# Optimization experiments

Hardware: AMD Instinct MI355X
Metric: run time of the kernel (lower is better)

Reference implementation:

```python
import jax, jax.numpy as jnp
import numpy as np

NEG_INF = -1.0e9  # matches torch code's masked fill value


def setup_inputs() -> dict:
    key = jax.random.key(0)
    k1, k2, k3, k4 = jax.random.split(key, 4)
    n, q, s, d, v = 8, 4096, 4096, 64, 64
    return {
        "queries_nqd": jax.random.normal(k1, (n, q, d), dtype=jnp.float32),
        "keys_nsd": jax.random.normal(k2, (n, s, d), dtype=jnp.float32),
        "values_nsv": jax.random.normal(k3, (n, s, v), dtype=jnp.float32),
        "attention_mask_nqs": jax.random.randint(k4, (n, q, s), 0, 2).astype(jnp.bool_),
    }


def reference(queries_nqd, keys_nsd, values_nsv, attention_mask_nqs):
    d = queries_nqd.shape[-1]
    scale = 1.0 / jnp.sqrt(jnp.asarray(d, dtype=queries_nqd.dtype))
    # [n,q,s] = [n,q,d] @ [n,d,s]
    scores_nqs = jnp.einsum("nqd,nsd->nqs", queries_nqd, keys_nsd) * scale
    scores_nqs = jnp.where(attention_mask_nqs, scores_nqs, jnp.asarray(NEG_INF, scores_nqs.dtype))
    probs_nqs = jax.nn.softmax(scores_nqs, axis=-1)
    # dropout p=0.0 (eval) -> identity
    return jnp.einsum("nqs,nsv->nqv", probs_nqs, values_nsv)
```

## Files before the change

### kernel.cpp

```cpp
#include <hip/hip_runtime.h>
#include <hip/hip_bf16.h>


#define NHEADS 8
#define QLEN   4096
#define SLEN   4096
#define DDIM   64
#define VDIM   64
#define SBLK   64
#define QBLK   128
#define NCHUNK (SLEN / SBLK)

typedef __bf16          bf16x4 __attribute__((ext_vector_type(4)));
typedef __bf16          bf16x8 __attribute__((ext_vector_type(8)));
typedef float           f32x4  __attribute__((ext_vector_type(4)));
typedef float           f32x16 __attribute__((ext_vector_type(16)));
typedef unsigned int    u32x4  __attribute__((ext_vector_type(4)));
typedef unsigned short  u16x4  __attribute__((ext_vector_type(4)));

#define KSWZ(s) (((s) & 7) << 4)
#define VSWZ(v) ((((v) >> 2) & 7) << 4)
#define PSWZ(q) (((q) & 3) << 4)
#define CLAMPC(c) ((c) < NCHUNK ? (c) : NCHUNK - 1)

#define LDS_BARRIER() do {                                          \
  asm volatile("s_waitcnt lgkmcnt(0)" ::: "memory");                \
  __builtin_amdgcn_s_barrier();                                     \
  __builtin_amdgcn_sched_barrier(0);                                \
} while (0)

__device__ __forceinline__ f32x16 zero16() {
  f32x16 z;
#pragma unroll
  for (int i = 0; i < 16; ++i) z[i] = 0.f;
  return z;
}

__device__ __forceinline__ int detect_mfmt(const unsigned char* __restrict__ M) {
  const int lane = threadIdx.x & 63;
  u32x4 w = *((const u32x4*)M + lane);
  unsigned o = w[0] | w[1] | w[2] | w[3];
  unsigned comb = ((o & 0x00FFFF00u) ? 1u : 0u) | ((o & 0x000000FFu) ? 2u : 0u);
  comb |= __shfl_xor((int)comb, 1);  comb |= __shfl_xor((int)comb, 2);
  comb |= __shfl_xor((int)comb, 4);  comb |= __shfl_xor((int)comb, 8);
  comb |= __shfl_xor((int)comb, 16); comb |= __shfl_xor((int)comb, 32);
  return ((comb & 1u) == 0u) ? 1 : (((comb & 2u) == 0u) ? 2 : 0);
}

template<bool U8>
__global__ __launch_bounds__(512, 2)
void attn_fwd(const float* __restrict__ Qg, const float* __restrict__ Kg,
              const float* __restrict__ Vg, const unsigned char* __restrict__ Mg,
              float* __restrict__ Og)
{
  __shared__ __align__(16) unsigned short Ksh[2][64 * 64];
  __shared__ __align__(16) unsigned short Vsh[2][64 * 64];
  __shared__ __align__(16) unsigned short Psh[8][32 * 32];
  __shared__ __align__(16) float mO[4][32][68];
  __shared__            float mM[4][2][32];

  {
    const int mfmt = detect_mfmt(Mg);
    if (U8 ? (mfmt != 0) : (mfmt == 0)) return;
  }

  const int tid   = threadIdx.x;
  const int wave  = tid >> 6;
  const int lane  = tid & 63;
  const int qtile = wave & 3;
  const int shalf = wave >> 2;
  const int lq    = lane & 31;
  const int h     = lane >> 5;

  const int head = blockIdx.x;
  const int qblk = blockIdx.y;

  const float* Qp = Qg + ((size_t)head * QLEN + (size_t)qblk * QBLK) * DDIM;
  const float* Kp = Kg + (size_t)head * SLEN * DDIM;
  const float* Vp = Vg + (size_t)head * SLEN * VDIM;
  float* Op = Og + ((size_t)head * QLEN + (size_t)qblk * QBLK) * DDIM;

  const float QSCALE = 0.125f * 1.44269504f;
  const int qrow = qtile * 32 + lq;
  bf16x8 qf[4];
#pragma unroll
  for (int kd = 0; kd < 4; ++kd) {
    const float* qp = Qp + (size_t)qrow * DDIM + 16 * kd + 8 * h;
    f32x4 a = *(const f32x4*)qp;
    f32x4 b = *(const f32x4*)(qp + 4);
    bf16x8 t;
#pragma unroll
    for (int j = 0; j < 4; ++j) { t[j] = (__bf16)(a[j] * QSCALE); t[4 + j] = (__bf16)(b[j] * QSCALE); }
    qf[kd] = t;
  }

  const size_t mbase = ((size_t)head * QLEN + (size_t)qblk * QBLK + qrow) * SLEN
                     + (size_t)shalf * 32;
  const unsigned char* mrow8  = Mg + mbase;
  const unsigned*      mrow32 = (const unsigned*)Mg + mbase;

  f32x16 oacc[2];
  oacc[0] = zero16(); oacc[1] = zero16();
  float m_run = -INFINITY;
  float l_run = 0.f;

  f32x4 kpA[2], vpA[2], kpB[2], vpB[2];
  unsigned m8A[4],  m8B[4];
  u32x4    m32A[4], m32B[4];

#define PREFETCH_KV(C, KP, VP)                                                 \
  _Pragma("unroll")                                                            \
  for (int it = 0; it < 2; ++it) {                                             \
    int srow = (tid >> 4) + it * 32;                                           \
    int d0   = (tid & 15) * 4;                                                 \
    size_t gs = (size_t)(CLAMPC(C) * SBLK + srow);                             \
    KP[it] = *(const f32x4*)(Kp + gs * DDIM + d0);                             \
    VP[it] = *(const f32x4*)(Vp + gs * VDIM + d0);                             \
  }

#define WRITE_KV(BUF, KP, VP)                                                  \
  _Pragma("unroll")                                                            \
  for (int it = 0; it < 2; ++it) {                                             \
    int srow = (tid >> 4) + it * 32;                                           \
    int d0   = (tid & 15) * 4;                                                 \
    bf16x4 kb;                                                                 \
    _Pragma("unroll") for (int j = 0; j < 4; ++j) kb[j] = (__bf16)KP[it][j];   \
    int koff = (srow * 128 + d0 * 2) ^ KSWZ(srow);                             \
    *(u16x4*)((char*)Ksh[BUF] + koff) = __builtin_bit_cast(u16x4, kb);         \
    _Pragma("unroll")                                                          \
    for (int j = 0; j < 4; ++j) {                                              \
      int v = d0 + j;                                                          \
      unsigned short b = __builtin_bit_cast(unsigned short, (__bf16)VP[it][j]); \
      int voff = (v * 128 + srow * 2) ^ VSWZ(v);                               \
      *(unsigned short*)((char*)Vsh[BUF] + voff) = b;                          \
    }                                                                          \
  }

#define LOAD_MASK(M8, M32, C)                                                  \
  if constexpr (U8) {                                                          \
    _Pragma("unroll")                                                          \
    for (int st = 0; st < 4; ++st)                                             \
      M8[st] = *(const unsigned*)(mrow8 + (size_t)CLAMPC(C) * SBLK + 8 * st + 4 * h); \
  } else {                                                                     \
    _Pragma("unroll")                                                          \
    for (int st = 0; st < 4; ++st)                                             \
      M32[st] = *(const u32x4*)(mrow32 + (size_t)CLAMPC(C) * SBLK + 8 * st + 4 * h); \
  }

#define CHUNK_BODY(C, CUR, KPF, VPF, KPW, VPW, M8U, M32U) {                    \
  PREFETCH_KV((C) + 2, KPF, VPF);                                              \
       \
  f32x16 sacc = zero16();                                                      \
  __builtin_amdgcn_s_setprio(1);                                               \
  _Pragma("unroll")                                                            \
  for (int kd = 0; kd < 4; ++kd) {                                             \
    int srow = shalf * 32 + lq;                                                \
    int off = (srow * 128 + (32 * kd + 16 * h)) ^ KSWZ(srow);                  \
    bf16x8 kf = *(const bf16x8*)((const char*)Ksh[CUR] + off);                 \
    sacc = __builtin_amdgcn_mfma_f32_32x32x16_bf16(kf, qf[kd], sacc, 0, 0, 0); \
  }                                                                            \
  __builtin_amdgcn_s_setprio(0);                                               \
               \
  float vals[4][4];                                                            \
  float mloc = -INFINITY;                                                      \
  _Pragma("unroll")                                                            \
  for (int st = 0; st < 4; ++st) {                                             \
    bool keep[4];                                                              \
    if constexpr (U8) {                                                        \
      _Pragma("unroll")                                                        \
      for (int r = 0; r < 4; ++r) keep[r] = ((M8U[st] >> (8 * r)) & 0xFFu) != 0u; \
    } else {                                                                   \
      _Pragma("unroll")                                                        \
      for (int r = 0; r < 4; ++r) keep[r] = M32U[st][r] != 0u;                 \
    }                                                                          \
    _Pragma("unroll")                                                          \
    for (int r = 0; r < 4; ++r) {                                              \
      float v = keep[r] ? sacc[4 * st + r] : -1.0e9f;                          \
      vals[st][r] = v;                                                         \
      mloc = fmaxf(mloc, v);                                                   \
    }                                                                          \
  }                                                                            \
  LOAD_MASK(M8U, M32U, (C) + 2);            \
  mloc = fmaxf(mloc, __shfl_xor(mloc, 32));                                    \
      \
  if (!__all(mloc <= m_run + 8.0f)) {                                          \
    float m_new = fmaxf(m_run, mloc);                                          \
    float alpha = __builtin_amdgcn_exp2f(m_run - m_new);                       \
    l_run *= alpha;                                                            \
    _Pragma("unroll")                                                          \
    for (int vt = 0; vt < 2; ++vt) {                                           \
      _Pragma("unroll")                                                        \
      for (int r = 0; r < 16; ++r) oacc[vt][r] *= alpha;                       \
    }                                                                          \
    m_run = m_new;                                                             \
  }                                                                            \
  float lsum = 0.f;                                                            \
  _Pragma("unroll")                                                            \
  for (int st = 0; st < 4; ++st) {                                             \
    bf16x4 pb;                                                                 \
    _Pragma("unroll")                                                          \
    for (int r = 0; r < 4; ++r) {                                              \
      float p = __builtin_amdgcn_exp2f(vals[st][r] - m_run);                   \
      lsum += p;                                                               \
      pb[r] = (__bf16)p;                                                       \
    }                                                                          \
    int poff = (lq * 64 + (16 * st + 8 * h)) ^ PSWZ(lq);                       \
    *(unsigned long long*)((char*)Psh[wave] + poff) =                          \
        __builtin_bit_cast(unsigned long long, pb);                            \
  }                                                                            \
  lsum += __shfl_xor(lsum, 32);                                                \
  l_run += lsum;                                                               \
               \
  __builtin_amdgcn_s_setprio(1);                                               \
  _Pragma("unroll")                                                            \
  for (int ks2 = 0; ks2 < 2; ++ks2) {                                          \
    int poff = (lq * 64 + (32 * ks2 + 16 * h)) ^ PSWZ(lq);                     \
    bf16x8 pf = *(const bf16x8*)((const char*)Psh[wave] + poff);               \
    _Pragma("unroll")                                                          \
    for (int vt = 0; vt < 2; ++vt) {                                           \
      int vrow = vt * 32 + lq;                                                 \
      int voff = (vrow * 128 + (64 * shalf + 32 * ks2 + 16 * h)) ^ VSWZ(vrow); \
      bf16x8 vf = *(const bf16x8*)((const char*)Vsh[CUR] + voff);              \
      oacc[vt] = __builtin_amdgcn_mfma_f32_32x32x16_bf16(vf, pf, oacc[vt], 0, 0, 0); \
    }                                                                          \
  }                                                                            \
  __builtin_amdgcn_s_setprio(0);                                               \
  WRITE_KV((CUR) ^ 1, KPW, VPW);         \
  LDS_BARRIER();                                                               \
}

  PREFETCH_KV(0, kpA, vpA);
  LOAD_MASK(m8A, m32A, 0);
  PREFETCH_KV(1, kpB, vpB);
  LOAD_MASK(m8B, m32B, 1);
  WRITE_KV(0, kpA, vpA);
  LDS_BARRIER();

  for (int cc = 0; cc < NCHUNK; cc += 2) {
    CHUNK_BODY(cc,     0, kpA, vpA, kpB, vpB, m8A, m32A);
    CHUNK_BODY(cc + 1, 1, kpB, vpB, kpA, vpA, m8B, m32B);
  }

  if (shalf == 1) {
#pragma unroll
    for (int vt = 0; vt < 2; ++vt) {
#pragma unroll
      for (int st = 0; st < 4; ++st) {
        int v0 = 32 * vt + 8 * st + 4 * h;
        f32x4 o;
#pragma unroll
        for (int r = 0; r < 4; ++r) o[r] = oacc[vt][4 * st + r];
        *(f32x4*)&mO[qtile][lq][v0] = o;
      }
    }
    if (h == 0) {
      mM[qtile][0][lq] = m_run;
      mM[qtile][1][lq] = l_run;
    }
  }
  LDS_BARRIER();
  if (shalf == 0) {
    float m1 = mM[qtile][0][lq];
    float l1 = mM[qtile][1][lq];
    float mm = fmaxf(m_run, m1);
    float a0 = __builtin_amdgcn_exp2f(m_run - mm);
    float a1 = __builtin_amdgcn_exp2f(m1 - mm);
    float inv = 1.0f / (l_run * a0 + l1 * a1);
    float* orow = Op + (size_t)qrow * VDIM;
#pragma unroll
    for (int vt = 0; vt < 2; ++vt) {
#pragma unroll
      for (int st = 0; st < 4; ++st) {
        int v0 = 32 * vt + 8 * st + 4 * h;
        f32x4 o1 = *(const f32x4*)&mO[qtile][lq][v0];
        f32x4 o;
#pragma unroll
        for (int r = 0; r < 4; ++r) o[r] = (oacc[vt][4 * st + r] * a0 + o1[r] * a1) * inv;
        *(f32x4*)(orow + v0) = o;
      }
    }
  }
#undef PREFETCH_KV
#undef WRITE_KV
#undef LOAD_MASK
#undef CHUNK_BODY
}

extern "C" void kernel_launch(void* const* d_in, const int* in_sizes, int n_in,
                              void* d_out, int out_size, void* d_ws, size_t ws_size,
                              hipStream_t stream) {
  const float* Qg = (const float*)d_in[0];
  const float* Kg = (const float*)d_in[1];
  const float* Vg = (const float*)d_in[2];
  const unsigned char* Mg = (const unsigned char*)d_in[3];
  float* Og = (float*)d_out;

  dim3 grid(NHEADS, QLEN / QBLK);
  dim3 block(512);
  attn_fwd<true ><<<grid, block, 0, stream>>>(Qg, Kg, Vg, Mg, Og);
  attn_fwd<false><<<grid, block, 0, stream>>>(Qg, Kg, Vg, Mg, Og);
}
```

Baseline: 150.2 us.

## Process 128-key phases and pass P through cross-lane shuffles instead of LDS

Doubles the per-phase key block to 128, so each barrier covers two 32-key tiles per wave and the number of LDS barriers and K/V staging rounds is halved. The softmax probabilities are packed into bf16 pairs and exchanged between lane halves with __shfl_xor to build the MFMA B operand directly, removing the per-wave P scratch buffer in LDS. The final merge buffers reuse the K/V shared arrays. The cost is more registers (8 prefetched K/V vectors and 8 mask words per buffer) and a shallower prefetch distance of one phase instead of two chunks, which could reduce occupancy or expose load latency.

```diff
diff --git a/kernel.cpp b/kernel.cpp
--- a/kernel.cpp
+++ b/kernel.cpp
@@ -7,9 +7,9 @@
 #define SLEN   4096
 #define DDIM   64
 #define VDIM   64
-#define SBLK   64
+#define PBLK   128
 #define QBLK   128
-#define NCHUNK (SLEN / SBLK)
+#define NPHASE (SLEN / PBLK)
 
 typedef __bf16          bf16x4 __attribute__((ext_vector_type(4)));
 typedef __bf16          bf16x8 __attribute__((ext_vector_type(8)));
@@ -20,8 +20,7 @@
 
 #define KSWZ(s) (((s) & 7) << 4)
 #define VSWZ(v) ((((v) >> 2) & 7) << 4)
-#define PSWZ(q) (((q) & 3) << 4)
-#define CLAMPC(c) ((c) < NCHUNK ? (c) : NCHUNK - 1)
+#define CLAMPP(p) ((p) < NPHASE ? (p) : NPHASE - 1)
 
 #define LDS_BARRIER() do {                                          \
   asm volatile("s_waitcnt lgkmcnt(0)" ::: "memory");                \
@@ -34,6 +33,13 @@
 #pragma unroll
   for (int i = 0; i < 16; ++i) z[i] = 0.f;
   return z;
+}
+
+__device__ __forceinline__ unsigned short bfb(float x) {
+  return __builtin_bit_cast(unsigned short, (__bf16)x);
+}
+__device__ __forceinline__ unsigned pk2(float a, float b) {
+  return (unsigned)bfb(a) | ((unsigned)bfb(b) << 16);
 }
 
 __device__ __forceinline__ int detect_mfmt(const unsigned char* __restrict__ M) {
@@ -53,11 +59,8 @@
               const float* __restrict__ Vg, const unsigned char* __restrict__ Mg,
               float* __restrict__ Og)
 {
-  __shared__ __align__(16) unsigned short Ksh[2][64 * 64];
-  __shared__ __align__(16) unsigned short Vsh[2][64 * 64];
-  __shared__ __align__(16) unsigned short Psh[8][32 * 32];
-  __shared__ __align__(16) float mO[4][32][68];
-  __shared__            float mM[4][2][32];
+  __shared__ __align__(16) unsigned short Ksh[2][128 * 64];
+  __shared__ __align__(16) unsigned short Vsh[2][64 * 128];
 
   {
     const int mfmt = detect_mfmt(Mg);
@@ -94,8 +97,7 @@
     qf[kd] = t;
   }
 
-  const size_t mbase = ((size_t)head * QLEN + (size_t)qblk * QBLK + qrow) * SLEN
-                     + (size_t)shalf * 32;
+  const size_t mbase = ((size_t)head * QLEN + (size_t)qblk * QBLK + qrow) * SLEN;
   const unsigned char* mrow8  = Mg + mbase;
   const unsigned*      mrow32 = (const unsigned*)Mg + mbase;
 
@@ -104,74 +106,87 @@
   float m_run = -INFINITY;
   float l_run = 0.f;
 
-  f32x4 kpA[2], vpA[2], kpB[2], vpB[2];
-  unsigned m8A[4],  m8B[4];
-  u32x4    m32A[4], m32B[4];
-
-#define PREFETCH_KV(C, KP, VP)                                                 \
-  _Pragma("unroll")                                                            \
-  for (int it = 0; it < 2; ++it) {                                             \
-    int srow = (tid >> 4) + it * 32;                                           \
-    int d0   = (tid & 15) * 4;                                                 \
-    size_t gs = (size_t)(CLAMPC(C) * SBLK + srow);                             \
-    KP[it] = *(const f32x4*)(Kp + gs * DDIM + d0);                             \
-    VP[it] = *(const f32x4*)(Vp + gs * VDIM + d0);                             \
-  }
-
-#define WRITE_KV(BUF, KP, VP)                                                  \
-  _Pragma("unroll")                                                            \
-  for (int it = 0; it < 2; ++it) {                                             \
-    int srow = (tid >> 4) + it * 32;                                           \
+  f32x4 kp0, kp1, kp2, kp3, vp0, vp1, vp2, vp3;
+  unsigned m8A[8],  m8B[8];
+  u32x4    m32A[8], m32B[8];
+
+#define PREFETCH_KV(P)                                                         \
+  {                                                                            \
+    size_t b_ = (size_t)CLAMPP(P) * PBLK;                                      \
+    int sr_ = tid >> 4, d0_ = (tid & 15) * 4;                                  \
+    kp0 = *(const f32x4*)(Kp + (b_ + sr_     ) * DDIM + d0_);                  \
+    kp1 = *(const f32x4*)(Kp + (b_ + sr_ + 32) * DDIM + d0_);                  \
+    kp2 = *(const f32x4*)(Kp + (b_ + sr_ + 64) * DDIM + d0_);                  \
+    kp3 = *(const f32x4*)(Kp + (b_ + sr_ + 96) * DDIM + d0_);                  \
+    vp0 = *(const f32x4*)(Vp + (b_ + sr_     ) * VDIM + d0_);                  \
+    vp1 = *(const f32x4*)(Vp + (b_ + sr_ + 32) * VDIM + d0_);                  \
+    vp2 = *(const f32x4*)(Vp + (b_ + sr_ + 64) * VDIM + d0_);                  \
+    vp3 = *(const f32x4*)(Vp + (b_ + sr_ + 96) * VDIM + d0_);                  \
+  }
+
+#define WRITE_ONE(BUF, KP, VP, IT)                                             \
+  {                                                                            \
+    int srow = (tid >> 4) + (IT) * 32;                                         \
     int d0   = (tid & 15) * 4;                                                 \
     bf16x4 kb;                                                                 \
-    _Pragma("unroll") for (int j = 0; j < 4; ++j) kb[j] = (__bf16)KP[it][j];   \
+    _Pragma("unroll") for (int j = 0; j < 4; ++j) kb[j] = (__bf16)KP[j];       \
     int koff = (srow * 128 + d0 * 2) ^ KSWZ(srow);                             \
     *(u16x4*)((char*)Ksh[BUF] + koff) = __builtin_bit_cast(u16x4, kb);         \
     _Pragma("unroll")                                                          \
     for (int j = 0; j < 4; ++j) {                                              \
       int v = d0 + j;                                                          \
-      unsigned short b = __builtin_bit_cast(unsigned short, (__bf16)VP[it][j]); \
-      int voff = (v * 128 + srow * 2) ^ VSWZ(v);                               \
+      unsigned short b = __builtin_bit_cast(unsigned short, (__bf16)VP[j]);    \
+      int voff = (v * 256 + srow * 2) ^ VSWZ(v);                               \
       *(unsigned short*)((char*)Vsh[BUF] + voff) = b;                          \
     }                                                                          \
   }
 
-#define LOAD_MASK(M8, M32, C)                                                  \
+#define WRITE_KV(BUF)                                                          \
+  WRITE_ONE(BUF, kp0, vp0, 0) WRITE_ONE(BUF, kp1, vp1, 1)                      \
+  WRITE_ONE(BUF, kp2, vp2, 2) WRITE_ONE(BUF, kp3, vp3, 3)
+
+#define LOAD_MASK(M8, M32, P)                                                  \
   if constexpr (U8) {                                                          \
     _Pragma("unroll")                                                          \
-    for (int st = 0; st < 4; ++st)                                             \
-      M8[st] = *(const unsigned*)(mrow8 + (size_t)CLAMPC(C) * SBLK + 8 * st + 4 * h); \
+    for (int st2 = 0; st2 < 2; ++st2)                                          \
+      _Pragma("unroll")                                                        \
+      for (int st = 0; st < 4; ++st)                                           \
+        M8[4 * st2 + st] = *(const unsigned*)(mrow8 + (size_t)CLAMPP(P) * PBLK \
+                           + 64 * shalf + 32 * st2 + 8 * st + 4 * h);          \
   } else {                                                                     \
     _Pragma("unroll")                                                          \
-    for (int st = 0; st < 4; ++st)                                             \
-      M32[st] = *(const u32x4*)(mrow32 + (size_t)CLAMPC(C) * SBLK + 8 * st + 4 * h); \
-  }
-
-#define CHUNK_BODY(C, CUR, KPF, VPF, KPW, VPW, M8U, M32U) {                    \
-  PREFETCH_KV((C) + 2, KPF, VPF);                                              \
-       \
+    for (int st2 = 0; st2 < 2; ++st2)                                          \
+      _Pragma("unroll")                                                        \
+      for (int st = 0; st < 4; ++st)                                           \
+        M32[4 * st2 + st] = *(const u32x4*)(mrow32 + (size_t)CLAMPP(P) * PBLK  \
+                           + 64 * shalf + 32 * st2 + 8 * st + 4 * h);          \
+  }
+
+#define TILE(CUR, ST2, MU8, MU32) {                                            \
+                       \
   f32x16 sacc = zero16();                                                      \
+  int srow_ = 64 * shalf + 32 * (ST2) + lq;                                    \
   __builtin_amdgcn_s_setprio(1);                                               \
   _Pragma("unroll")                                                            \
   for (int kd = 0; kd < 4; ++kd) {                                             \
-    int srow = shalf * 32 + lq;                                                \
-    int off = (srow * 128 + (32 * kd + 16 * h)) ^ KSWZ(srow);                  \
+    int off = (srow_ * 128 + (32 * kd + 16 * h)) ^ KSWZ(srow_);                \
     bf16x8 kf = *(const bf16x8*)((const char*)Ksh[CUR] + off);                 \
     sacc = __builtin_amdgcn_mfma_f32_32x32x16_bf16(kf, qf[kd], sacc, 0, 0, 0); \
   }                                                                            \
   __builtin_amdgcn_s_setprio(0);                                               \
-               \
+                     \
   float vals[4][4];                                                            \
   float mloc = -INFINITY;                                                      \
   _Pragma("unroll")                                                            \
   for (int st = 0; st < 4; ++st) {                                             \
     bool keep[4];                                                              \
     if constexpr (U8) {                                                        \
-      _Pragma("unroll")                                                        \
-      for (int r = 0; r < 4; ++r) keep[r] = ((M8U[st] >> (8 * r)) & 0xFFu) != 0u; \
+      unsigned w_ = MU8[4 * (ST2) + st];                                       \
+      _Pragma("unroll")                                                        \
+      for (int r = 0; r < 4; ++r) keep[r] = ((w_ >> (8 * r)) & 0xFFu) != 0u;   \
     } else {                                                                   \
       _Pragma("unroll")                                                        \
-      for (int r = 0; r < 4; ++r) keep[r] = M32U[st][r] != 0u;                 \
+      for (int r = 0; r < 4; ++r) keep[r] = MU32[4 * (ST2) + st][r] != 0u;     \
     }                                                                          \
     _Pragma("unroll")                                                          \
     for (int r = 0; r < 4; ++r) {                                              \
@@ -180,88 +195,102 @@
       mloc = fmaxf(mloc, v);                                                   \
     }                                                                          \
   }                                                                            \
-  LOAD_MASK(M8U, M32U, (C) + 2);            \
   mloc = fmaxf(mloc, __shfl_xor(mloc, 32));                                    \
-      \
-  if (!__all(mloc <= m_run + 8.0f)) {                                          \
+  if (!__all(mloc <= m_run + 8.0f)) {                   \
     float m_new = fmaxf(m_run, mloc);                                          \
     float alpha = __builtin_amdgcn_exp2f(m_run - m_new);                       \
     l_run *= alpha;                                                            \
     _Pragma("unroll")                                                          \
-    for (int vt = 0; vt < 2; ++vt) {                                           \
+    for (int vt = 0; vt < 2; ++vt)                                             \
       _Pragma("unroll")                                                        \
       for (int r = 0; r < 16; ++r) oacc[vt][r] *= alpha;                       \
-    }                                                                          \
     m_run = m_new;                                                             \
   }                                                                            \
+                 \
   float lsum = 0.f;                                                            \
+  unsigned wlo[4], whi[4];                                                     \
   _Pragma("unroll")                                                            \
   for (int st = 0; st < 4; ++st) {                                             \
-    bf16x4 pb;                                                                 \
-    _Pragma("unroll")                                                          \
-    for (int r = 0; r < 4; ++r) {                                              \
-      float p = __builtin_amdgcn_exp2f(vals[st][r] - m_run);                   \
-      lsum += p;                                                               \
-      pb[r] = (__bf16)p;                                                       \
-    }                                                                          \
-    int poff = (lq * 64 + (16 * st + 8 * h)) ^ PSWZ(lq);                       \
-    *(unsigned long long*)((char*)Psh[wave] + poff) =                          \
-        __builtin_bit_cast(unsigned long long, pb);                            \
+    float p0 = __builtin_amdgcn_exp2f(vals[st][0] - m_run);                    \
+    float p1 = __builtin_amdgcn_exp2f(vals[st][1] - m_run);                    \
+    float p2 = __builtin_amdgcn_exp2f(vals[st][2] - m_run);                    \
+    float p3 = __builtin_amdgcn_exp2f(vals[st][3] - m_run);                    \
+    lsum += (p0 + p1) + (p2 + p3);                                             \
+    wlo[st] = pk2(p0, p1);                                                     \
+    whi[st] = pk2(p2, p3);                                                     \
   }                                                                            \
   lsum += __shfl_xor(lsum, 32);                                                \
   l_run += lsum;                                                               \
-               \
-  __builtin_amdgcn_s_setprio(1);                                               \
+   \
+   \
+   \
   _Pragma("unroll")                                                            \
   for (int ks2 = 0; ks2 < 2; ++ks2) {                                          \
-    int poff = (lq * 64 + (32 * ks2 + 16 * h)) ^ PSWZ(lq);                     \
-    bf16x8 pf = *(const bf16x8*)((const char*)Psh[wave] + poff);               \
+    unsigned slo = h ? wlo[2 * ks2] : wlo[2 * ks2 + 1];    \
+    unsigned shi = h ? whi[2 * ks2] : whi[2 * ks2 + 1];                        \
+    unsigned rlo = __shfl_xor(slo, 32);                                        \
+    unsigned rhi = __shfl_xor(shi, 32);                                        \
+    unsigned klo = h ? wlo[2 * ks2 + 1] : wlo[2 * ks2];    \
+    unsigned khi = h ? whi[2 * ks2 + 1] : whi[2 * ks2];                        \
+    u32x4 fw;                                                                  \
+    fw[0] = h ? rlo : klo;  fw[1] = h ? rhi : khi;                             \
+    fw[2] = h ? klo : rlo;  fw[3] = h ? khi : rhi;                             \
+    bf16x8 pf = __builtin_bit_cast(bf16x8, fw);                                \
+    __builtin_amdgcn_s_setprio(1);                                             \
     _Pragma("unroll")                                                          \
     for (int vt = 0; vt < 2; ++vt) {                                           \
-      int vrow = vt * 32 + lq;                                                 \
-      int voff = (vrow * 128 + (64 * shalf + 32 * ks2 + 16 * h)) ^ VSWZ(vrow); \
+      int vrow = 32 * vt + lq;                                                 \
+      int voff = (vrow * 256 + (128 * shalf + 64 * (ST2) + 32 * ks2 + 16 * h)) \
+                 ^ VSWZ(vrow);                                                 \
       bf16x8 vf = *(const bf16x8*)((const char*)Vsh[CUR] + voff);              \
       oacc[vt] = __builtin_amdgcn_mfma_f32_32x32x16_bf16(vf, pf, oacc[vt], 0, 0, 0); \
     }                                                                          \
-  }                                                                            \
-  __builtin_amdgcn_s_setprio(0);                                               \
-  WRITE_KV((CUR) ^ 1, KPW, VPW);         \
+    __builtin_amdgcn_s_setprio(0);                                             \
+  }                                                                            \
+}
+
+#define PHASE_BODY(P, CUR, MU8, MU32, ML8, ML32) {                             \
+  PREFETCH_KV((P) + 1);                                                        \
+  LOAD_MASK(ML8, ML32, (P) + 1);                                               \
+  TILE(CUR, 0, MU8, MU32);                                                     \
+  TILE(CUR, 1, MU8, MU32);                                                     \
+  WRITE_KV((CUR) ^ 1);                                                         \
   LDS_BARRIER();                                                               \
 }
 
-  PREFETCH_KV(0, kpA, vpA);
+  PREFETCH_KV(0);
   LOAD_MASK(m8A, m32A, 0);
-  PREFETCH_KV(1, kpB, vpB);
-  LOAD_MASK(m8B, m32B, 1);
-  WRITE_KV(0, kpA, vpA);
+  WRITE_KV(0);
   LDS_BARRIER();
 
-  for (int cc = 0; cc < NCHUNK; cc += 2) {
-    CHUNK_BODY(cc,     0, kpA, vpA, kpB, vpB, m8A, m32A);
-    CHUNK_BODY(cc + 1, 1, kpB, vpB, kpA, vpA, m8B, m32B);
-  }
-
+  for (int pp = 0; pp < NPHASE; pp += 2) {
+    PHASE_BODY(pp,     0, m8A, m32A, m8B, m32B);
+    PHASE_BODY(pp + 1, 1, m8B, m32B, m8A, m32A);
+  }
+
+  float* mO = (float*)&Ksh[0][0];
+  float* mM = (float*)&Vsh[0][0];
   if (shalf == 1) {
 #pragma unroll
     for (int vt = 0; vt < 2; ++vt) {
 #pragma unroll
       for (int st = 0; st < 4; ++st) {
-        int v0 = 32 * vt + 8 * st + 4 * h;
-        f32x4 o;
-#pragma unroll
-        for (int r = 0; r < 4; ++r) o[r] = oacc[vt][4 * st + r];
-        *(f32x4*)&mO[qtile][lq][v0] = o;
+#pragma unroll
+        for (int r = 0; r < 4; ++r) {
+          int v = 32 * vt + 8 * st + 4 * h + r;
+          mO[((size_t)qtile * 64 + v) * 32 + lq] = oacc[vt][4 * st + r];
+        }
       }
     }
     if (h == 0) {
-      mM[qtile][0][lq] = m_run;
-      mM[qtile][1][lq] = l_run;
+      mM[(qtile * 2 + 0) * 32 + lq] = m_run;
+      mM[(qtile * 2 + 1) * 32 + lq] = l_run;
     }
   }
   LDS_BARRIER();
   if (shalf == 0) {
-    float m1 = mM[qtile][0][lq];
-    float l1 = mM[qtile][1][lq];
+    float m1 = mM[(qtile * 2 + 0) * 32 + lq];
+    float l1 = mM[(qtile * 2 + 1) * 32 + lq];
     float mm = fmaxf(m_run, m1);
     float a0 = __builtin_amdgcn_exp2f(m_run - mm);
     float a1 = __builtin_amdgcn_exp2f(m1 - mm);
@@ -272,18 +301,22 @@
 #pragma unroll
       for (int st = 0; st < 4; ++st) {
         int v0 = 32 * vt + 8 * st + 4 * h;
-        f32x4 o1 = *(const f32x4*)&mO[qtile][lq][v0];
         f32x4 o;
 #pragma unroll
-        for (int r = 0; r < 4; ++r) o[r] = (oacc[vt][4 * st + r] * a0 + o1[r] * a1) * inv;
+        for (int r = 0; r < 4; ++r) {
+          float o1 = mO[((size_t)qtile * 64 + v0 + r) * 32 + lq];
+          o[r] = (oacc[vt][4 * st + r] * a0 + o1 * a1) * inv;
+        }
         *(f32x4*)(orow + v0) = o;
       }
     }
   }
 #undef PREFETCH_KV
+#undef WRITE_ONE
 #undef WRITE_KV
 #undef LOAD_MASK
-#undef CHUNK_BODY
+#undef TILE
+#undef PHASE_BODY
 }
 
 extern "C" void kernel_launch(void* const* d_in, const int* in_sizes, int n_in,
```

New measurement: 158.2 us. +5.3%, slower.
